# Kernel tuning notes

Hardware: AMD Instinct MI355X
Metric: run time of the kernel (lower is better)

The kernel has to match this reference:

```python
import jax, jax.numpy as jnp
import numpy as np

# ---- static config (from xib add_argument defaults / chosen production sizes) ----
B, L = 16, 50            # batch, text length
LU, KU, DIM = 60, 100, 60
V, MAXVL = 2000, 10      # vocab size, max vocab word length (J)
MIN_WL, MAX_WL = 4, 10   # min/max extracted word length
NE = MAX_WL - MIN_WL + 1 # number of len_e candidates
INS_DEL_COST = 3.5       # min_ins_del_cost
UNEXTRACTED_PROB = 0.01
CONTEXT_WEIGHT = 0.1     # weight for context (conv) log-probs
NEG = -9999.9


def setup_inputs() -> dict:
    key = jax.random.key(0)
    ks = jax.random.split(key, 8)
    unit_id_seqs = jax.random.randint(ks[0], (B, L), 0, LU)
    lengths = 10 + jax.random.randint(ks[1], (B,), 0, L - 9)  # in [10, L]
    unit_repr = jax.random.normal(ks[2], (KU, DIM), jnp.float32)
    aligner_weight = 0.1 * jax.random.normal(ks[3], (LU, KU), jnp.float32)
    conv_w = jax.random.normal(ks[4], (DIM, DIM, 3), jnp.float32) / np.sqrt(3.0 * DIM)
    conv_b = jnp.zeros((DIM,), jnp.float32)
    vocab_ids = jax.random.randint(ks[5], (V, MAXVL), 0, KU)
    vocab_lengths = MIN_WL + jax.random.randint(ks[6], (V,), 0, MAXVL - MIN_WL + 1)
    return dict(unit_id_seqs=unit_id_seqs, lengths=lengths, unit_repr=unit_repr,
                aligner_weight=aligner_weight, conv_w=conv_w, conv_b=conv_b,
                vocab_ids=vocab_ids, vocab_lengths=vocab_lengths)


def reference(unit_id_seqs, lengths, unit_repr, aligner_weight, conv_w, conv_b,
              vocab_ids, vocab_lengths):
    # ---- G2P layer: embedding-as-matmul + Conv1d over length ----
    ku_char_repr = aligner_weight @ unit_repr                 # (LU, DIM)
    emb = ku_char_repr[unit_id_seqs]                          # (B, L, DIM)
    x = jnp.swapaxes(emb, 1, 2)                               # (B, DIM, L)
    y = jax.lax.conv_general_dilated(x, conv_w, (1,), 'SAME',
                                     dimension_numbers=('NCH', 'OIH', 'NCH'))
    word_repr = jnp.swapaxes(y + conv_b[None, :, None], 1, 2)  # (B, L, DIM)
    char_log_probs = jax.nn.log_softmax(ku_char_repr @ unit_repr.T, axis=-1)  # (LU, KU)
    alignment = jnp.exp(char_log_probs)
    ctx_log_probs = jax.nn.log_softmax(word_repr @ unit_repr.T, axis=-1)      # (B, L, KU)
    # per-position substitution log prob against each known unit
    pos_lp = char_log_probs[unit_id_seqs] + CONTEXT_WEIGHT * ctx_log_probs    # (B, L, KU)
    sub = pos_lp[:, :, vocab_ids]                                             # (B, L, V, J)
    sub = jnp.pad(sub, ((0, 0), (0, MAX_WL), (0, 0), (0, 0)), constant_values=NEG)
    J = MAXVL
    # ---- edit-distance style DP over (span char i, vocab char j), vectorized
    # over (batch, start position, vocab). prev[b,s,j,v] = f[i-1][j].
    j_ar = jnp.arange(J + 1, dtype=sub.dtype)
    prev = jnp.broadcast_to((-INS_DEL_COST * j_ar)[None, None, :, None], (B, L, J + 1, V))
    vl_idx = jnp.broadcast_to(vocab_lengths[None, None, None, :].astype(jnp.int32), (B, L, 1, V))
    lls = []
    for i in range(1, MAX_WL + 1):          # fixed small loop (<=10)
        sub_i = sub[:, i - 1:i - 1 + L]     # (B, L, V, J): char at position s+i-1
        row = [jnp.full((B, L, V), -INS_DEL_COST * i, dtype=sub.dtype)]
        for j in range(1, J + 1):           # fixed small loop (<=10)
            diag = prev[:, :, j - 1, :] + sub_i[:, :, :, j - 1]
            up = prev[:, :, j, :] - INS_DEL_COST
            left = row[j - 1] - INS_DEL_COST
            row.append(jnp.maximum(diag, jnp.maximum(up, left)))
        prev = jnp.stack(row, axis=2)       # (B, L, J+1, V)
        if i >= MIN_WL:                     # matched ll for word length i
            lls.append(jnp.take_along_axis(prev, vl_idx, axis=2)[:, :, 0, :])
    ll = jnp.stack(lls, axis=2)             # (B, L, NE, V) = matches.ll
    # ---- viability mask + unextracted penalty, pick best candidate ----
    starts = jnp.arange(L)
    word_lens = MIN_WL + jnp.arange(NE)
    viable = (starts[None, :, None] + word_lens[None, None, :]) <= lengths[:, None, None]  # (B,L,NE)
    unextracted = (lengths[:, None, None] - word_lens[None, None, :]).astype(ll.dtype)     # (B,1,NE)
    score = (ll + jnp.where(viable, 0.0, NEG)[..., None]
             + (unextracted * np.log(UNEXTRACTED_PROB))[..., None, :, None][:, 0])
    flat = score.reshape(B, L * NE * V)
    best_idx = jnp.argmax(flat, axis=1)
    best_matched_ll = jnp.max(flat, axis=1)
    start = best_idx // (NE * V)
    e_idx = (best_idx // V) % NE
    best_matched_vocab = best_idx % V
    end = start + MIN_WL + e_idx - 1
    return start, end, best_matched_ll, best_matched_vocab, alignment
```

## Files before the change

### kernel.cpp

```cpp
#include <hip/hip_runtime.h>
#include <math.h>
#include <stdint.h>

#define B_ 16
#define L_ 50
#define LU_ 60
#define KU_ 100
#define DIM_ 60
#define V_ 2000
#define MAXVL_ 10
#define MIN_WL_ 4
#define MAX_WL_ 10
#define NE_ 7
#define IDC_ 3.5f
#define LOG_UNEXT_ (-4.6051701859880913680359829093687f)
#define CTXW_ 0.1f
#define NQ_ 13

#define WS_PLP  0
#define WS_BEST_BYTES (80000u * 4u)
#define BEST_STRIDE 8
#define WS_VPACK_BYTES (WS_BEST_BYTES + 1024u)

#define URP_ 61
#define CWP_ 61
#define TSP_ 12

__global__ __launch_bounds__(256) void ctx_kernel(
    const int* __restrict__ uid,
    const float* __restrict__ unit_repr,
    const float* __restrict__ aligner_w,
    const float* __restrict__ conv_w,
    const float* __restrict__ conv_b,
    const int* __restrict__ vocab_ids,
    const int* __restrict__ vocab_lengths,
    float* __restrict__ ws_plp,
    float* __restrict__ out_align,
    unsigned long long* __restrict__ g_best,
    int* __restrict__ vpack)
{
  int blk = blockIdx.x;
  int t = threadIdx.x;

  if (blk == B_ * NQ_) {
    __shared__ unsigned cnt[NE_];
    if (t < NE_) cnt[t] = 0u;
    __syncthreads();
    for (int v = t; v < V_; v += 256)
      atomicAdd(&cnt[vocab_lengths[v] - MIN_WL_], 1u);
    __syncthreads();
    if (t == 0) {
      unsigned s = 0;
      for (int e = 0; e < NE_; ++e) { unsigned c = cnt[e]; cnt[e] = s; s += c; }
    }
    __syncthreads();
    for (int v = t; v < V_; v += 256) {
      int vl = vocab_lengths[v];
      unsigned dst = atomicAdd(&cnt[vl - MIN_WL_], 1u);
      unsigned q0 = 0u, q1 = 0u, q2 = 0u;
#pragma unroll
      for (int j = 0; j < 4; ++j) q0 |= ((unsigned)vocab_ids[v * MAXVL_ + j]) << (j * 8);
#pragma unroll
      for (int j = 0; j < 4; ++j) q1 |= ((unsigned)vocab_ids[v * MAXVL_ + 4 + j]) << (j * 8);
#pragma unroll
      for (int j = 0; j < 2; ++j) q2 |= ((unsigned)vocab_ids[v * MAXVL_ + 8 + j]) << (j * 8);
      int4 w;
      w.x = (int)q0; w.y = (int)q1; w.z = (int)q2;
      w.w = (int)((unsigned)vl | ((unsigned)v << 8));
      ((int4*)vpack)[dst] = w;
    }
    return;
  }

  int b = blk / NQ_, q = blk % NQ_;
  int l0 = 4 * q;
  int npos = (l0 + 4 <= L_) ? 4 : (L_ - l0);
  int alr = (blk < LU_) ? blk : -1;

  __shared__ float s_ur[KU_ * URP_];
  __shared__ float s_cw[3 * DIM_ * CWP_];
  __shared__ float s_aw[7 * KU_];
  __shared__ float s_kx[7 * DIM_];
  __shared__ float swr[4 * DIM_];
  __shared__ float sclp[4 * KU_];
  __shared__ float sctx[4 * KU_];
  __shared__ float salg[KU_];
  __shared__ float sls[9];

  if (blk == 0 && t < B_) g_best[t * BEST_STRIDE] = 0ull;

  const float4* ur4 = (const float4*)unit_repr;
  for (int k = t; k < (KU_ * DIM_) / 4; k += 256) {
    float4 v = ur4[k];
    int i0 = 4 * k;
    s_ur[((i0 + 0) / DIM_) * URP_ + ((i0 + 0) % DIM_)] = v.x;
    s_ur[((i0 + 1) / DIM_) * URP_ + ((i0 + 1) % DIM_)] = v.y;
    s_ur[((i0 + 2) / DIM_) * URP_ + ((i0 + 2) % DIM_)] = v.z;
    s_ur[((i0 + 3) / DIM_) * URP_ + ((i0 + 3) % DIM_)] = v.w;
  }
  const float4* cw4 = (const float4*)conv_w;
  for (int k = t; k < (DIM_ * DIM_ * 3) / 4; k += 256) {
    float4 v = cw4[k];
    int i0 = 4 * k;
    float vv[4] = {v.x, v.y, v.z, v.w};
#pragma unroll
    for (int e = 0; e < 4; ++e) {
      int idx = i0 + e;
      int o = idx / (3 * DIM_), id = idx % (3 * DIM_);
      s_cw[id * CWP_ + o] = vv[e];
    }
  }
  for (int i = t; i < 7 * KU_; i += 256) {
    int m = i / KU_, k = i - m * KU_;
    float w = 0.f;
    if (m < 6) {
      int ld = l0 - 1 + m;
      if (ld >= 0 && ld < L_) {
        int u = uid[b * L_ + ld];
        w = aligner_w[u * KU_ + k];
      }
    } else if (alr >= 0) {
      w = aligner_w[alr * KU_ + k];
    }
    s_aw[i] = w;
  }
  __syncthreads();

  for (int idx = t; idx < 7 * DIM_; idx += 256) {
    int m = idx / DIM_, c = idx - m * DIM_;
    const float4* aw4 = (const float4*)&s_aw[m * KU_];
    float acc = 0.f;
    for (int k4 = 0; k4 < KU_ / 4; ++k4) {
      float4 a = aw4[k4];
      int k = 4 * k4;
      acc += a.x * s_ur[(k + 0) * URP_ + c];
      acc += a.y * s_ur[(k + 1) * URP_ + c];
      acc += a.z * s_ur[(k + 2) * URP_ + c];
      acc += a.w * s_ur[(k + 3) * URP_ + c];
    }
    s_kx[idx] = acc;
  }
  __syncthreads();

  for (int idx = t; idx < 240 + 4 * KU_; idx += 256) {
    if (idx < 240) {
      int p = idx / DIM_, o = idx - p * DIM_;
      const float4* x04 = (const float4*)&s_kx[(p + 0) * DIM_];
      const float4* x14 = (const float4*)&s_kx[(p + 1) * DIM_];
      const float4* x24 = (const float4*)&s_kx[(p + 2) * DIM_];
      float acc = conv_b[o];
      for (int i4 = 0; i4 < DIM_ / 4; ++i4) {
        float4 x0 = x04[i4], x1 = x14[i4], x2 = x24[i4];
        int i = 4 * i4;
        acc += x0.x * s_cw[((i + 0) * 3 + 0) * CWP_ + o];
        acc += x1.x * s_cw[((i + 0) * 3 + 1) * CWP_ + o];
        acc += x2.x * s_cw[((i + 0) * 3 + 2) * CWP_ + o];
        acc += x0.y * s_cw[((i + 1) * 3 + 0) * CWP_ + o];
        acc += x1.y * s_cw[((i + 1) * 3 + 1) * CWP_ + o];
        acc += x2.y * s_cw[((i + 1) * 3 + 2) * CWP_ + o];
        acc += x0.z * s_cw[((i + 2) * 3 + 0) * CWP_ + o];
        acc += x1.z * s_cw[((i + 2) * 3 + 1) * CWP_ + o];
        acc += x2.z * s_cw[((i + 2) * 3 + 2) * CWP_ + o];
        acc += x0.w * s_cw[((i + 3) * 3 + 0) * CWP_ + o];
        acc += x1.w * s_cw[((i + 3) * 3 + 1) * CWP_ + o];
        acc += x2.w * s_cw[((i + 3) * 3 + 2) * CWP_ + o];
      }
      swr[p * DIM_ + o] = acc;
    } else {
      int r = idx - 240;
      int p = r / KU_, j = r - p * KU_;
      const float4* kx4 = (const float4*)&s_kx[(p + 1) * DIM_];
      float acc = 0.f;
      for (int d4 = 0; d4 < DIM_ / 4; ++d4) {
        float4 x = kx4[d4];
        int d = 4 * d4;
        acc += x.x * s_ur[j * URP_ + d + 0];
        acc += x.y * s_ur[j * URP_ + d + 1];
        acc += x.z * s_ur[j * URP_ + d + 2];
        acc += x.w * s_ur[j * URP_ + d + 3];
      }
      sclp[r] = acc;
    }
  }
  __syncthreads();

  for (int idx = t; idx < 4 * KU_ + KU_; idx += 256) {
    if (idx < 4 * KU_) {
      int p = idx / KU_, j = idx - p * KU_;
      const float4* w4 = (const float4*)&swr[p * DIM_];
      float acc = 0.f;
      for (int d4 = 0; d4 < DIM_ / 4; ++d4) {
        float4 x = w4[d4];
        int d = 4 * d4;
        acc += x.x * s_ur[j * URP_ + d + 0];
        acc += x.y * s_ur[j * URP_ + d + 1];
        acc += x.z * s_ur[j * URP_ + d + 2];
        acc += x.w * s_ur[j * URP_ + d + 3];
      }
      sctx[idx] = acc;
    } else {
      int j = idx - 4 * KU_;
      const float4* kx4 = (const float4*)&s_kx[6 * DIM_];
      float acc = 0.f;
      for (int d4 = 0; d4 < DIM_ / 4; ++d4) {
        float4 x = kx4[d4];
        int d = 4 * d4;
        acc += x.x * s_ur[j * URP_ + d + 0];
        acc += x.y * s_ur[j * URP_ + d + 1];
        acc += x.z * s_ur[j * URP_ + d + 2];
        acc += x.w * s_ur[j * URP_ + d + 3];
      }
      salg[j] = acc;
    }
  }
  __syncthreads();

  {
    int g = t >> 5, lane = t & 31;
#pragma unroll
    for (int round = 0; round < 2; ++round) {
      int r = round * 8 + g;
      if (r < 9) {
        const float* arr = (r == 8) ? salg
                          : ((r & 1) ? &sctx[(r >> 1) * KU_] : &sclp[(r >> 1) * KU_]);
        float v1 = arr[lane];
        float v2 = arr[32 + lane];
        float v3 = arr[64 + lane];
        float v4 = (lane < KU_ - 96) ? arr[96 + lane] : -1e30f;
        float mx = fmaxf(fmaxf(v1, v2), fmaxf(v3, v4));
#pragma unroll
        for (int off = 16; off > 0; off >>= 1)
          mx = fmaxf(mx, __shfl_xor(mx, off));
        float s = expf(v1 - mx) + expf(v2 - mx) + expf(v3 - mx) +
                  ((lane < KU_ - 96) ? expf(v4 - mx) : 0.f);
#pragma unroll
        for (int off = 16; off > 0; off >>= 1)
          s += __shfl_xor(s, off);
        if (lane == 0) sls[r] = mx + logf(s);
      }
    }
  }
  __syncthreads();

  for (int idx = t; idx < 4 * KU_; idx += 256) {
    int p = idx / KU_, j = idx - p * KU_;
    if (p < npos) {
      float pos = (sclp[idx] - sls[2 * p]) + CTXW_ * (sctx[idx] - sls[2 * p + 1]);
      ws_plp[(b * L_ + l0 + p) * KU_ + j] = pos;
    }
  }
  if (alr >= 0 && t < KU_)
    out_align[alr * KU_ + t] = expf(salg[t] - sls[8]);
}

__global__ __launch_bounds__(256) void dp_kernel(
    const int* __restrict__ lengths,
    const float* __restrict__ ws_plp,
    const int* __restrict__ vpack,
    unsigned long long* __restrict__ g_best)
{
  int bl = blockIdx.x;
  int b = bl / L_, l = bl % L_;
  int len_b = lengths[b];
  int imax = len_b - l;
  if (imax > MAX_WL_) imax = MAX_WL_;
  if (imax < MIN_WL_) return;

  __shared__ float sT[KU_ * TSP_];
  __shared__ unsigned long long swave[4];
  int t = threadIdx.x;
  {
    int n = imax * KU_;
    for (int idx = t; idx < n; idx += 256) {
      int i = idx / KU_, k = idx - i * KU_;
      sT[k * TSP_ + i] = ws_plp[(bl + i) * KU_ + k];
    }
  }
  __syncthreads();

  int p = blockIdx.y * 256 + t;
  const int4* vp4 = (const int4*)vpack;
  int4 w0 = (2 * p < V_) ? vp4[2 * p] : make_int4(0, 0, 0, 0);
  int4 w1 = (2 * p + 1 < V_) ? vp4[2 * p + 1] : make_int4(0, 0, 0, 0);
  unsigned p0[3] = {(unsigned)w0.x, (unsigned)w0.y, (unsigned)w0.z};
  unsigned p1[3] = {(unsigned)w1.x, (unsigned)w1.y, (unsigned)w1.z};
  int vlen0 = (int)((unsigned)w0.w & 0xFFu);
  int vlen1 = (int)((unsigned)w1.w & 0xFFu);
  int v0 = (int)(((unsigned)w0.w) >> 8);
  int v1 = (int)(((unsigned)w1.w) >> 8);
  int jmax = (vlen0 > vlen1) ? vlen0 : vlen1;

  float A0[MAXVL_ + 1], A1[MAXVL_ + 1];
#pragma unroll
  for (int i = 0; i <= MAXVL_; ++i) {
    A0[i] = -IDC_ * (float)i;
    A1[i] = A0[i];
  }
  unsigned long long bestKey = 0ull;

#pragma unroll
  for (int j = 1; j <= MAXVL_; ++j) {
    if (j <= jmax) {
      int k0 = (int)((p0[(j - 1) >> 2] >> (((j - 1) & 3) * 8)) & 0xFFu);
      int k1 = (int)((p1[(j - 1) >> 2] >> (((j - 1) & 3) * 8)) & 0xFFu);
      const float* c0 = &sT[k0 * TSP_];
      const float* c1 = &sT[k1 * TSP_];
      float4 a0 = *(const float4*)(c0);
      float4 m0 = *(const float4*)(c0 + 4);
      float2 e0 = *(const float2*)(c0 + 8);
      float4 a1 = *(const float4*)(c1);
      float4 m1 = *(const float4*)(c1 + 4);
      float2 e1 = *(const float2*)(c1 + 8);
      float s0[MAXVL_] = {a0.x, a0.y, a0.z, a0.w, m0.x, m0.y, m0.z, m0.w, e0.x, e0.y};
      float s1[MAXVL_] = {a1.x, a1.y, a1.z, a1.w, m1.x, m1.y, m1.z, m1.w, e1.x, e1.y};
      float B0[MAXVL_ + 1], B1[MAXVL_ + 1];
      B0[0] = -IDC_ * (float)j;
      B1[0] = B0[0];
#pragma unroll
      for (int i = 1; i <= MAXVL_; ++i) {
        B0[i] = fmaxf(A0[i - 1] + s0[i - 1], fmaxf(A0[i], B0[i - 1]) - IDC_);
        B1[i] = fmaxf(A1[i - 1] + s1[i - 1], fmaxf(A1[i], B1[i - 1]) - IDC_);
      }
      if (j == vlen0) {
#pragma unroll
        for (int e = 0; e < NE_; ++e) {
          int i = MIN_WL_ + e;
          if (i <= imax) {
            float score = B0[i] + (float)(len_b - i) * LOG_UNEXT_;
            unsigned int idx = (unsigned int)(l * (NE_ * V_) + e * V_ + v0);
            unsigned int u = __float_as_uint(score);
            u = (u & 0x80000000u) ? ~u : (u | 0x80000000u);
            unsigned long long key =
                ((unsigned long long)u << 32) | (unsigned long long)(~idx);
            if (key > bestKey) bestKey = key;
          }
        }
      }
      if (j == vlen1) {
#pragma unroll
        for (int e = 0; e < NE_; ++e) {
          int i = MIN_WL_ + e;
          if (i <= imax) {
            float score = B1[i] + (float)(len_b - i) * LOG_UNEXT_;
            unsigned int idx = (unsigned int)(l * (NE_ * V_) + e * V_ + v1);
            unsigned int u = __float_as_uint(score);
            u = (u & 0x80000000u) ? ~u : (u | 0x80000000u);
            unsigned long long key =
                ((unsigned long long)u << 32) | (unsigned long long)(~idx);
            if (key > bestKey) bestKey = key;
          }
        }
      }
#pragma unroll
      for (int i = 0; i <= MAXVL_; ++i) { A0[i] = B0[i]; A1[i] = B1[i]; }
    }
  }

#pragma unroll
  for (int off = 32; off > 0; off >>= 1) {
    unsigned long long o = __shfl_down(bestKey, off);
    if (o > bestKey) bestKey = o;
  }
  int wid = t >> 6;
  if ((t & 63) == 0) swave[wid] = bestKey;
  __syncthreads();
  if (t == 0) {
    unsigned long long k0 = swave[0];
    for (int w = 1; w < 4; ++w)
      if (swave[w] > k0) k0 = swave[w];
    atomicMax(g_best + (size_t)b * BEST_STRIDE, k0);
  }
}

__global__ void decode_kernel(const unsigned long long* __restrict__ g_best,
                              float* __restrict__ out)
{
  int t = threadIdx.x;
  if (t < B_) {
    unsigned long long key = g_best[t * BEST_STRIDE];
    unsigned int u = (unsigned int)(key >> 32);
    unsigned int idx = ~((unsigned int)(key & 0xFFFFFFFFull));
    unsigned int bits = (u & 0x80000000u) ? (u & 0x7FFFFFFFu) : ~u;
    float val = __uint_as_float(bits);
    int start = (int)(idx / (NE_ * V_));
    int rem = (int)(idx % (NE_ * V_));
    int e = rem / V_;
    int vv = rem % V_;
    out[t] = (float)start;
    out[B_ + t] = (float)(start + MIN_WL_ + e - 1);
    out[2 * B_ + t] = val;
    out[3 * B_ + t] = (float)vv;
  }
}

extern "C" void kernel_launch(void* const* d_in, const int* in_sizes, int n_in,
                              void* d_out, int out_size, void* d_ws, size_t ws_size,
                              hipStream_t stream)
{
  const int* uid            = (const int*)d_in[0];
  const int* lengths        = (const int*)d_in[1];
  const float* unit_repr    = (const float*)d_in[2];
  const float* aligner_w    = (const float*)d_in[3];
  const float* conv_w       = (const float*)d_in[4];
  const float* conv_b       = (const float*)d_in[5];
  const int* vocab_ids      = (const int*)d_in[6];
  const int* vocab_lengths  = (const int*)d_in[7];
  float* out = (float*)d_out;
  float* ws_f = (float*)d_ws;
  unsigned long long* g_best =
      (unsigned long long*)((char*)d_ws + WS_BEST_BYTES);
  int* vpack = (int*)((char*)d_ws + WS_VPACK_BYTES);

  ctx_kernel<<<B_ * NQ_ + 1, 256, 0, stream>>>(uid, unit_repr, aligner_w,
                                               conv_w, conv_b, vocab_ids,
                                               vocab_lengths, ws_f + WS_PLP,
                                               out + 4 * B_, g_best, vpack);
  dim3 g3(B_ * L_, 4);
  dp_kernel<<<g3, 256, 0, stream>>>(lengths, ws_f + WS_PLP, vpack, g_best);
  decode_kernel<<<1, 64, 0, stream>>>(g_best, out);
}
```

Baseline: 102.5 us.

## Swap DP loop order and stage plp rows directly in shared memory

The DP kernel now loads the per-position log-prob rows into shared memory as contiguous float4 copies, with no transposed gather, padding each row to 104 floats. The edit-distance recurrence is reordered so the outer loop runs over text length i and the inner loop over vocab position j, with each step reading one scalar per token. Vocab token offsets are unpacked once up front, and the best score per vocab word is tracked as a float plus index instead of building a 64-bit key inside the loop. This removes the strided transpose on load and the repeated key construction, but adds more scattered scalar LDS reads and relies on the per-thread best being combined correctly with ties.

Result: slower. 125.8 us (+22.8%).

```diff
diff --git a/kernel.cpp b/kernel.cpp
--- a/kernel.cpp
+++ b/kernel.cpp
@@ -24,7 +24,7 @@
 
 #define URP_ 61
 #define CWP_ 61
-#define TSP_ 12
+#define RKP_ 104
 
 __global__ __launch_bounds__(256) void ctx_kernel(
     const int* __restrict__ uid,
@@ -43,20 +43,20 @@
   int t = threadIdx.x;
 
   if (blk == B_ * NQ_) {
-    __shared__ unsigned cnt[NE_];
-    if (t < NE_) cnt[t] = 0u;
+    __shared__ unsigned scnt[NE_];
+    if (t < NE_) scnt[t] = 0u;
     __syncthreads();
     for (int v = t; v < V_; v += 256)
-      atomicAdd(&cnt[vocab_lengths[v] - MIN_WL_], 1u);
+      atomicAdd(&scnt[vocab_lengths[v] - MIN_WL_], 1u);
     __syncthreads();
     if (t == 0) {
       unsigned s = 0;
-      for (int e = 0; e < NE_; ++e) { unsigned c = cnt[e]; cnt[e] = s; s += c; }
+      for (int e = 0; e < NE_; ++e) { unsigned c = scnt[e]; scnt[e] = s; s += c; }
     }
     __syncthreads();
     for (int v = t; v < V_; v += 256) {
       int vl = vocab_lengths[v];
-      unsigned dst = atomicAdd(&cnt[vl - MIN_WL_], 1u);
+      unsigned dst = atomicAdd(&scnt[vl - MIN_WL_], 1u);
       unsigned q0 = 0u, q1 = 0u, q2 = 0u;
 #pragma unroll
       for (int j = 0; j < 4; ++j) q0 |= ((unsigned)vocab_ids[v * MAXVL_ + j]) << (j * 8);
@@ -266,15 +266,14 @@
   if (imax > MAX_WL_) imax = MAX_WL_;
   if (imax < MIN_WL_) return;
 
-  __shared__ float sT[KU_ * TSP_];
+  __shared__ float srow[MAX_WL_ * RKP_];
   __shared__ unsigned long long swave[4];
   int t = threadIdx.x;
-  {
-    int n = imax * KU_;
-    for (int idx = t; idx < n; idx += 256) {
-      int i = idx / KU_, k = idx - i * KU_;
-      sT[k * TSP_ + i] = ws_plp[(bl + i) * KU_ + k];
-    }
+  if (t < 250) {
+    const float4* src = (const float4*)(ws_plp + (size_t)bl * KU_);
+    int r = t / 25, m = t - r * 25;
+    float4 v = src[r * 25 + m];
+    *(float4*)&srow[r * RKP_ + 4 * m] = v;
   }
   __syncthreads();
 
@@ -282,78 +281,80 @@
   const int4* vp4 = (const int4*)vpack;
   int4 w0 = (2 * p < V_) ? vp4[2 * p] : make_int4(0, 0, 0, 0);
   int4 w1 = (2 * p + 1 < V_) ? vp4[2 * p + 1] : make_int4(0, 0, 0, 0);
-  unsigned p0[3] = {(unsigned)w0.x, (unsigned)w0.y, (unsigned)w0.z};
-  unsigned p1[3] = {(unsigned)w1.x, (unsigned)w1.y, (unsigned)w1.z};
   int vlen0 = (int)((unsigned)w0.w & 0xFFu);
   int vlen1 = (int)((unsigned)w1.w & 0xFFu);
   int v0 = (int)(((unsigned)w0.w) >> 8);
   int v1 = (int)(((unsigned)w1.w) >> 8);
   int jmax = (vlen0 > vlen1) ? vlen0 : vlen1;
 
+  int koff0[MAXVL_], koff1[MAXVL_];
+  {
+    unsigned q0[3] = {(unsigned)w0.x, (unsigned)w0.y, (unsigned)w0.z};
+    unsigned q1[3] = {(unsigned)w1.x, (unsigned)w1.y, (unsigned)w1.z};
+#pragma unroll
+    for (int j = 0; j < MAXVL_; ++j) {
+      koff0[j] = (int)((q0[j >> 2] >> ((j & 3) * 8)) & 0xFFu) * 4;
+      koff1[j] = (int)((q1[j >> 2] >> ((j & 3) * 8)) & 0xFFu) * 4;
+    }
+  }
+
   float A0[MAXVL_ + 1], A1[MAXVL_ + 1];
 #pragma unroll
   for (int i = 0; i <= MAXVL_; ++i) {
     A0[i] = -IDC_ * (float)i;
     A1[i] = A0[i];
   }
-  unsigned long long bestKey = 0ull;
-
-#pragma unroll
-  for (int j = 1; j <= MAXVL_; ++j) {
-    if (j <= jmax) {
-      int k0 = (int)((p0[(j - 1) >> 2] >> (((j - 1) & 3) * 8)) & 0xFFu);
-      int k1 = (int)((p1[(j - 1) >> 2] >> (((j - 1) & 3) * 8)) & 0xFFu);
-      const float* c0 = &sT[k0 * TSP_];
-      const float* c1 = &sT[k1 * TSP_];
-      float4 a0 = *(const float4*)(c0);
-      float4 m0 = *(const float4*)(c0 + 4);
-      float2 e0 = *(const float2*)(c0 + 8);
-      float4 a1 = *(const float4*)(c1);
-      float4 m1 = *(const float4*)(c1 + 4);
-      float2 e1 = *(const float2*)(c1 + 8);
-      float s0[MAXVL_] = {a0.x, a0.y, a0.z, a0.w, m0.x, m0.y, m0.z, m0.w, e0.x, e0.y};
-      float s1[MAXVL_] = {a1.x, a1.y, a1.z, a1.w, m1.x, m1.y, m1.z, m1.w, e1.x, e1.y};
-      float B0[MAXVL_ + 1], B1[MAXVL_ + 1];
-      B0[0] = -IDC_ * (float)j;
-      B1[0] = B0[0];
-#pragma unroll
-      for (int i = 1; i <= MAXVL_; ++i) {
-        B0[i] = fmaxf(A0[i - 1] + s0[i - 1], fmaxf(A0[i], B0[i - 1]) - IDC_);
-        B1[i] = fmaxf(A1[i - 1] + s1[i - 1], fmaxf(A1[i], B1[i - 1]) - IDC_);
-      }
-      if (j == vlen0) {
-#pragma unroll
-        for (int e = 0; e < NE_; ++e) {
-          int i = MIN_WL_ + e;
-          if (i <= imax) {
-            float score = B0[i] + (float)(len_b - i) * LOG_UNEXT_;
-            unsigned int idx = (unsigned int)(l * (NE_ * V_) + e * V_ + v0);
-            unsigned int u = __float_as_uint(score);
-            u = (u & 0x80000000u) ? ~u : (u | 0x80000000u);
-            unsigned long long key =
-                ((unsigned long long)u << 32) | (unsigned long long)(~idx);
-            if (key > bestKey) bestKey = key;
+
+  float bestSc0 = -1e30f, bestSc1 = -1e30f;
+  int bestI0 = 0, bestI1 = 0;
+  const char* sbase = (const char*)srow;
+
+#pragma unroll
+  for (int i = 1; i <= MAX_WL_; ++i) {
+    float b0 = -IDC_ * (float)i;
+    float b1 = b0;
+    float ci = (float)(len_b - i) * LOG_UNEXT_;
+    bool iok = (i <= imax);
+#pragma unroll
+    for (int j = 1; j <= MAXVL_; ++j) {
+      if (j <= jmax) {
+        float s0 = *(const float*)(sbase + (i - 1) * (RKP_ * 4) + koff0[j - 1]);
+        float s1 = *(const float*)(sbase + (i - 1) * (RKP_ * 4) + koff1[j - 1]);
+        float n0 = fmaxf(A0[j - 1] + s0, fmaxf(A0[j] - IDC_, b0 - IDC_));
+        float n1 = fmaxf(A1[j - 1] + s1, fmaxf(A1[j] - IDC_, b1 - IDC_));
+        A0[j - 1] = b0; A1[j - 1] = b1;
+        b0 = n0; b1 = n1;
+        if (i >= MIN_WL_) {
+          if (iok && j == vlen0) {
+            float sc = n0 + ci;
+            if (sc > bestSc0) { bestSc0 = sc; bestI0 = i; }
+          }
+          if (iok && j == vlen1) {
+            float sc = n1 + ci;
+            if (sc > bestSc1) { bestSc1 = sc; bestI1 = i; }
           }
         }
-      }
-      if (j == vlen1) {
-#pragma unroll
-        for (int e = 0; e < NE_; ++e) {
-          int i = MIN_WL_ + e;
-          if (i <= imax) {
-            float score = B1[i] + (float)(len_b - i) * LOG_UNEXT_;
-            unsigned int idx = (unsigned int)(l * (NE_ * V_) + e * V_ + v1);
-            unsigned int u = __float_as_uint(score);
-            u = (u & 0x80000000u) ? ~u : (u | 0x80000000u);
-            unsigned long long key =
-                ((unsigned long long)u << 32) | (unsigned long long)(~idx);
-            if (key > bestKey) bestKey = key;
-          }
-        }
-      }
-#pragma unroll
-      for (int i = 0; i <= MAXVL_; ++i) { A0[i] = B0[i]; A1[i] = B1[i]; }
-    }
+      } else if (j == jmax + 1) {
+        A0[j - 1] = b0; A1[j - 1] = b1;
+      }
+    }
+    if (jmax == MAXVL_) { A0[MAXVL_] = b0; A1[MAXVL_] = b1; }
+  }
+
+  unsigned long long bestKey = 0ull;
+  if (bestI0 > 0) {
+    unsigned int idx = (unsigned int)(l * (NE_ * V_) + (bestI0 - MIN_WL_) * V_ + v0);
+    unsigned int u = __float_as_uint(bestSc0);
+    u = (u & 0x80000000u) ? ~u : (u | 0x80000000u);
+    unsigned long long key = ((unsigned long long)u << 32) | (unsigned long long)(~idx);
+    if (key > bestKey) bestKey = key;
+  }
+  if (bestI1 > 0) {
+    unsigned int idx = (unsigned int)(l * (NE_ * V_) + (bestI1 - MIN_WL_) * V_ + v1);
+    unsigned int u = __float_as_uint(bestSc1);
+    u = (u & 0x80000000u) ? ~u : (u | 0x80000000u);
+    unsigned long long key = ((unsigned long long)u << 32) | (unsigned long long)(~idx);
+    if (key > bestKey) bestKey = key;
   }
 
 #pragma unroll
```
